# Optimization experiments

Measured on AMD Instinct MI355X. Metric: run time of the kernel, lower is better.

The kernel has to match this reference:

```python
import jax, jax.numpy as jnp
import numpy as np

N_GROUPS = 32  # getGroupSize(.) assumed -> channels // 8 (or //24 for 3*ch) == 32 for ch=256
HEADS = 4


def group_norm(x, gamma, beta, groups=N_GROUPS, eps=1e-5):
    n, c = x.shape
    xg = x.reshape(n, groups, c // groups)
    mu = xg.mean(-1, keepdims=True)
    var = xg.var(-1, keepdims=True)
    xn = ((xg - mu) * jax.lax.rsqrt(var + eps)).reshape(n, c)
    return xn * gamma + beta


def setup_inputs():
    key = jax.random.key(0)
    N, E, CH, HID = 2000, 16000, 256, 256
    ks = jax.random.split(key, 24)

    def w(k, shape, s=0.02):
        return (jax.random.normal(k, shape) * s).astype(jnp.float32)

    inp = {
        'x': jax.random.normal(ks[0], (N, CH), jnp.float32),
        'edge_index': jax.random.randint(ks[1], (2, E), 0, N),
        'edge_attr': jax.random.normal(ks[2], (E, CH), jnp.float32),
        # edge_mlp: GN(3ch)+ReLU -> Linear(3ch,hid) -> GN(hid)+ReLU -> Linear(hid,ch)
        'gn_e1_g': jnp.ones((3 * CH,), jnp.float32), 'gn_e1_b': jnp.zeros((3 * CH,), jnp.float32),
        'We1': w(ks[3], (3 * CH, HID)), 'be1': jnp.zeros((HID,), jnp.float32),
        'gn_e2_g': jnp.ones((HID,), jnp.float32), 'gn_e2_b': jnp.zeros((HID,), jnp.float32),
        'We2': w(ks[4], (HID, CH)), 'be2': jnp.zeros((CH,), jnp.float32),
        # actN: GN(ch)+ReLU
        'gn_n_g': jnp.ones((CH,), jnp.float32), 'gn_n_b': jnp.zeros((CH,), jnp.float32),
        # multi-head attention projections
        'Wq': w(ks[5], (CH, CH)), 'bq': jnp.zeros((CH,), jnp.float32),
        'Wk': w(ks[6], (CH, CH)), 'bk': jnp.zeros((CH,), jnp.float32),
        'Wv': w(ks[7], (CH, CH)), 'bv': jnp.zeros((CH,), jnp.float32),
        'Wo': w(ks[8], (CH, CH)), 'bo': jnp.zeros((CH,), jnp.float32),
        # node_mlp: Linear(2ch,hid) -> GN(hid)+ReLU -> Linear(hid,ch)
        'Wn1': w(ks[9], (2 * CH, HID)), 'bn1': jnp.zeros((HID,), jnp.float32),
        'gn_n2_g': jnp.ones((HID,), jnp.float32), 'gn_n2_b': jnp.zeros((HID,), jnp.float32),
        'Wn2': w(ks[10], (HID, CH)), 'bn2': jnp.zeros((CH,), jnp.float32),
    }
    return inp


def reference(x, edge_index, edge_attr,
              gn_e1_g, gn_e1_b, We1, be1, gn_e2_g, gn_e2_b, We2, be2,
              gn_n_g, gn_n_b, Wq, bq, Wk, bk, Wv, bv, Wo, bo,
              Wn1, bn1, gn_n2_g, gn_n2_b, Wn2, bn2):
    row, col = edge_index[0], edge_index[1]
    N, ch = x.shape
    E = edge_attr.shape[0]
    dk = ch // HEADS

    # ---- edge model: cat(src, tgt, e) -> GN/ReLU -> Lin -> GN/ReLU -> Lin (+res) ----
    e_in = jnp.concatenate([x[row], x[col], edge_attr], axis=1)  # [E, 3ch]
    h = jax.nn.relu(group_norm(e_in, gn_e1_g, gn_e1_b))
    h = h @ We1 + be1
    h = jax.nn.relu(group_norm(h, gn_e2_g, gn_e2_b))
    e_out = h @ We2 + be2 + edge_attr  # [E, ch]

    # ---- node model: dense-masked MHA, queries=nodes, keys/values=edges ----
    mask = jnp.zeros((N, E), x.dtype).at[col, jnp.arange(E)].set(1.0)  # scatter adjacency
    q = (x @ Wq + bq).reshape(N, HEADS, dk)
    k = (e_out @ Wk + bk).reshape(E, HEADS, dk)
    v = (e_out @ Wv + bv).reshape(E, HEADS, dk)
    scores = jnp.einsum('nhd,ehd->hne', q, k) / jnp.sqrt(jnp.float32(dk))  # [H, N, E]
    scores = jnp.where(mask[None] > 0, scores, jnp.float32(-1e9))
    attn = jax.nn.softmax(scores, axis=-1)
    g = jnp.einsum('hne,ehd->nhd', attn, v).reshape(N, ch) @ Wo + bo  # [N, ch]

    xa = jax.nn.relu(group_norm(x, gn_n_g, gn_n_b))
    h = jnp.concatenate([xa, g], axis=1) @ Wn1 + bn1  # thinker='cat'
    h = jax.nn.relu(group_norm(h, gn_n2_g, gn_n2_b))
    n_out = h @ Wn2 + bn2 + x  # residual

    return n_out, e_out
```

## Files before the change

kernel.cpp:

```cpp
#include <hip/hip_runtime.h>
#include <hip/hip_bf16.h>
#include <stdint.h>
#include <math.h>

#define CH 256

typedef __attribute__((ext_vector_type(8)))  short short8;
typedef __attribute__((ext_vector_type(16))) short short16;
typedef __attribute__((ext_vector_type(4)))  float f32x4;

#define GL2LDS16(g, l) __builtin_amdgcn_global_load_lds(                       \
    (const __attribute__((address_space(1))) void*)(g),                        \
    (__attribute__((address_space(3))) void*)(l), 16, 0, 0)

__device__ inline short f2bf(float f) {
    __hip_bfloat16 h = __float2bfloat16(f);
    short s;
    __builtin_memcpy(&s, &h, 2);
    return s;
}

__device__ inline float warp_sum64(float v) {
    v += __shfl_xor(v, 32, 64);
    v += __shfl_xor(v, 16, 64);
    v += __shfl_xor(v, 8, 64);
    v += __shfl_xor(v, 4, 64);
    v += __shfl_xor(v, 2, 64);
    v += __shfl_xor(v, 1, 64);
    return v;
}

template <int BM, int BN, int EPI, int VB>
__global__ __launch_bounds__(256) void mfma_gemm(
    const short* __restrict__ A, const short* __restrict__ Bt,
    const float* __restrict__ bias, const float* __restrict__ res,
    float* __restrict__ C, short* __restrict__ Cbf,
    const float* __restrict__ gamma, const float* __restrict__ beta,
    float* __restrict__ vbar,
    int M, int K, int Nc, int ldc, int coff)
{
    constexpr int BK = 32;
    constexpr int HM = BM / 2, HN = BN / 2;
    constexpr int FM = HM / 16, FN = HN / 16;
    constexpr int PA = (BM * BK) / (256 * 8);
    constexpr int PB = (BN * BK) / (256 * 8);
    __shared__ short As[BM * BK];
    __shared__ short Bs[BN * BK];

    const int t = threadIdx.x;
    const int wave = t >> 6, lane = t & 63;
    const int q = lane >> 4, l16 = lane & 15;
    const int row0 = blockIdx.y * BM;
    const int col0 = blockIdx.x * BN;
    const int wm = wave & 1, wn = wave >> 1;

    f32x4 acc[FM][FN];
    #pragma unroll
    for (int i = 0; i < FM; i++)
        #pragma unroll
        for (int j = 0; j < FN; j++) acc[i][j] = (f32x4){0.f, 0.f, 0.f, 0.f};

    for (int k0 = 0; k0 < K; k0 += BK) {
        #pragma unroll
        for (int p = 0; p < PA; p++) {
            int chunk = p * 256 + t;
            int r = chunk >> 2, ko = (chunk & 3) * 8;
            int gr = row0 + r; if (gr >= M) gr = M - 1;
            const short* gsrc = A + (size_t)gr * K + k0 + ko;
            short* ldst = &As[(p * 256 + wave * 64) * 8];
            GL2LDS16(gsrc, ldst);
        }
        #pragma unroll
        for (int p = 0; p < PB; p++) {
            int chunk = p * 256 + t;
            int r = chunk >> 2, ko = (chunk & 3) * 8;
            const short* gsrc = Bt + (size_t)(col0 + r) * K + k0 + ko;
            short* ldst = &Bs[(p * 256 + wave * 64) * 8];
            GL2LDS16(gsrc, ldst);
        }
        __syncthreads();
        short8 af[FM], bf[FN];
        #pragma unroll
        for (int mi = 0; mi < FM; mi++)
            af[mi] = *(const short8*)&As[(wm * HM + mi * 16 + l16) * BK + q * 8];
        #pragma unroll
        for (int ni = 0; ni < FN; ni++)
            bf[ni] = *(const short8*)&Bs[(wn * HN + ni * 16 + l16) * BK + q * 8];
        #pragma unroll
        for (int mi = 0; mi < FM; mi++)
            #pragma unroll
            for (int ni = 0; ni < FN; ni++)
                acc[mi][ni] = __builtin_amdgcn_mfma_f32_16x16x32_bf16(
                    af[mi], bf[ni], acc[mi][ni], 0, 0, 0);
        __syncthreads();
    }

    #pragma unroll
    for (int ni = 0; ni < FN; ni++) {
        int cg = col0 + wn * HN + ni * 16 + l16;
        float bv = bias[cg];
        if constexpr (EPI == 1) {
            float ga = gamma[cg], be = beta[cg];
            #pragma unroll
            for (int mi = 0; mi < FM; mi++) {
                #pragma unroll
                for (int r = 0; r < 4; r++) {
                    float v = acc[mi][ni][r] + bv;
                    float s = v, sq = v * v;
                    s += __shfl_xor(s, 1, 64);  sq += __shfl_xor(sq, 1, 64);
                    s += __shfl_xor(s, 2, 64);  sq += __shfl_xor(sq, 2, 64);
                    s += __shfl_xor(s, 4, 64);  sq += __shfl_xor(sq, 4, 64);
                    float mean = s * 0.125f;
                    float var = sq * 0.125f - mean * mean;
                    float o = fmaxf((v - mean) * rsqrtf(var + 1e-5f) * ga + be, 0.f);
                    int rg = row0 + wm * HM + mi * 16 + q * 4 + r;
                    if (rg < M) Cbf[(size_t)rg * ldc + coff + cg] = f2bf(o);
                }
            }
        } else {
            #pragma unroll
            for (int mi = 0; mi < FM; mi++) {
                #pragma unroll
                for (int r = 0; r < 4; r++) {
                    int rg = row0 + wm * HM + mi * 16 + q * 4 + r;
                    if (rg < M) {
                        float v = acc[mi][ni][r] + bv;
                        if (res) v += res[(size_t)rg * ldc + coff + cg];
                        if (C)   C[(size_t)rg * ldc + coff + cg] = v;
                        if (Cbf) Cbf[(size_t)rg * ldc + coff + cg] = f2bf(v);
                    }
                }
            }
            if constexpr (VB) {
                if (cg >= 256) {
                    float part = 0.f;
                    #pragma unroll
                    for (int mi = 0; mi < FM; mi++)
                        #pragma unroll
                        for (int r = 0; r < 4; r++) {
                            int rg = row0 + wm * HM + mi * 16 + q * 4 + r;
                            if (rg < M) part += acc[mi][ni][r] + bv;
                        }
                    part += __shfl_xor(part, 16, 64);
                    part += __shfl_xor(part, 32, 64);
                    if (q == 0) atomicAdd(&vbar[cg - 256], part);
                }
            }
        }
    }
}

struct WPack {
    const float* src[8];
    short* dst[8];
    int K[8];
    int start[8];
};

__global__ __launch_bounds__(256) void wconv_kernel(WPack p)
{
    int gk = blockIdx.x;
    int m = 0;
    #pragma unroll
    for (int i = 1; i < 8; i++) if (gk >= p.start[i]) m = i;
    int k0 = (gk - p.start[m]) * 16;
    int t = threadIdx.x;
    const float* src = p.src[m];
    short16 o;
    #pragma unroll
    for (int j = 0; j < 16; j++) o[j] = f2bf(src[(size_t)(k0 + j) * 256 + t]);
    *(short16*)(p.dst[m] + (size_t)t * p.K[m] + k0) = o;
}

__global__ __launch_bounds__(256) void prep_kernel(
    const float* __restrict__ x, short* __restrict__ x_bf,
    short* __restrict__ cat_bf,
    const float* __restrict__ gng, const float* __restrict__ gnb,
    float* __restrict__ vbar, const float* __restrict__ bk,
    const float* __restrict__ bv, float* __restrict__ bkv, int N)
{
    int t = threadIdx.x;
    if (blockIdx.x == 0) {
        vbar[t] = 0.f;
        bkv[t] = bk[t];
        bkv[256 + t] = bv[t];
    }
    int r = blockIdx.x * 8 + (t >> 5);
    int g = t & 31;
    if (r >= N) return;
    size_t xb = (size_t)r * CH + g * 8;
    float4 a = *(const float4*)&x[xb];
    float4 b = *(const float4*)&x[xb + 4];
    short8 xr;
    xr[0] = f2bf(a.x); xr[1] = f2bf(a.y); xr[2] = f2bf(a.z); xr[3] = f2bf(a.w);
    xr[4] = f2bf(b.x); xr[5] = f2bf(b.y); xr[6] = f2bf(b.z); xr[7] = f2bf(b.w);
    *(short8*)&x_bf[xb] = xr;
    float s  = a.x + a.y + a.z + a.w + b.x + b.y + b.z + b.w;
    float s2 = a.x*a.x + a.y*a.y + a.z*a.z + a.w*a.w
             + b.x*b.x + b.y*b.y + b.z*b.z + b.w*b.w;
    float m = s * 0.125f;
    float var = s2 * 0.125f - m * m;
    float rsd = rsqrtf(var + 1e-5f);
    float4 g0 = *(const float4*)&gng[g * 8];
    float4 g1 = *(const float4*)&gng[g * 8 + 4];
    float4 b0 = *(const float4*)&gnb[g * 8];
    float4 b1 = *(const float4*)&gnb[g * 8 + 4];
    short8 o;
    o[0] = f2bf(fmaxf((a.x - m) * rsd * g0.x + b0.x, 0.f));
    o[1] = f2bf(fmaxf((a.y - m) * rsd * g0.y + b0.y, 0.f));
    o[2] = f2bf(fmaxf((a.z - m) * rsd * g0.z + b0.z, 0.f));
    o[3] = f2bf(fmaxf((a.w - m) * rsd * g0.w + b0.w, 0.f));
    o[4] = f2bf(fmaxf((b.x - m) * rsd * g1.x + b1.x, 0.f));
    o[5] = f2bf(fmaxf((b.y - m) * rsd * g1.y + b1.y, 0.f));
    o[6] = f2bf(fmaxf((b.z - m) * rsd * g1.z + b1.z, 0.f));
    o[7] = f2bf(fmaxf((b.w - m) * rsd * g1.w + b1.w, 0.f));
    *(short8*)&cat_bf[(size_t)r * (2 * CH) + g * 8] = o;
}

__global__ __launch_bounds__(256) void build_ein_kernel(
    const float* __restrict__ x, const float* __restrict__ eattr,
    const int* __restrict__ rowi, const int* __restrict__ coli,
    const float* __restrict__ gng, const float* __restrict__ gnb,
    short* __restrict__ ein, int E)
{
    __shared__ float sb[768];
    __shared__ float smu[32], srs[32];
    int e = blockIdx.x, t = threadIdx.x;
    int r = rowi[e], c = coli[e];
    float v0 = x[(size_t)r * CH + t];
    float v1 = x[(size_t)c * CH + t];
    float v2 = eattr[(size_t)e * CH + t];
    sb[t] = v0; sb[256 + t] = v1; sb[512 + t] = v2;
    __syncthreads();
    if (t < 32) {
        float s = 0.f, s2 = 0.f;
        const float* p = &sb[t * 24];
        #pragma unroll
        for (int i = 0; i < 24; i++) { float v = p[i]; s += v; s2 += v * v; }
        float m = s * (1.f / 24.f);
        float var = s2 * (1.f / 24.f) - m * m;
        smu[t] = m; srs[t] = rsqrtf(var + 1e-5f);
    }
    __syncthreads();
    size_t base = (size_t)e * 768;
    #pragma unroll
    for (int j = 0; j < 3; j++) {
        int pos = j * 256 + t;
        int g = pos / 24;
        float v = (j == 0) ? v0 : (j == 1) ? v1 : v2;
        v = fmaxf((v - smu[g]) * srs[g] * gng[pos] + gnb[pos], 0.f);
        ein[base + pos] = f2bf(v);
    }
}

__global__ __launch_bounds__(1024) void csr_kernel(
    const int* __restrict__ coli, int* __restrict__ offsets,
    int* __restrict__ elist, int N, int E)
{
    __shared__ int cnt[2048];
    __shared__ int s[1024];
    int t = threadIdx.x;
    cnt[t] = 0; cnt[1024 + t] = 0;
    __syncthreads();
    for (int e = t; e < E; e += 1024) atomicAdd(&cnt[coli[e]], 1);
    __syncthreads();
    int a = (2 * t     < N) ? cnt[2 * t]     : 0;
    int b = (2 * t + 1 < N) ? cnt[2 * t + 1] : 0;
    s[t] = a + b;
    __syncthreads();
    for (int off = 1; off < 1024; off <<= 1) {
        int v = (t >= off) ? s[t - off] : 0;
        __syncthreads();
        s[t] += v;
        __syncthreads();
    }
    int excl = (t > 0) ? s[t - 1] : 0;
    if (2 * t < N)     { offsets[2 * t]     = excl;     cnt[2 * t]     = excl; }
    if (2 * t + 1 < N) { offsets[2 * t + 1] = excl + a; cnt[2 * t + 1] = excl + a; }
    if (t == 1023) offsets[N] = s[1023];
    __syncthreads();
    for (int e = t; e < E; e += 1024) {
        int p = atomicAdd(&cnt[coli[e]], 1);
        elist[p] = e;
    }
}

__global__ __launch_bounds__(256) void attn_kernel(
    const float* __restrict__ qb, const float* __restrict__ kv,
    const int* __restrict__ offsets, const int* __restrict__ elist,
    const float* __restrict__ vbar, short* __restrict__ g_bf, int N, int E)
{
    int n = blockIdx.x;
    int c = threadIdx.x;
    float qv = qb[(size_t)n * CH + c];
    int s0 = offsets[n], s1 = offsets[n + 1];
    float out;
    if (s1 > s0) {
        float m = -INFINITY, l = 0.f, num = 0.f;
        int e = elist[s0];
        float kc = kv[(size_t)e * 512 + c];
        float vc = kv[(size_t)e * 512 + 256 + c];
        for (int idx = s0; idx < s1; idx++) {
            float kcur = kc, vcur = vc;
            if (idx + 1 < s1) {
                int e2 = elist[idx + 1];
                kc = kv[(size_t)e2 * 512 + c];
                vc = kv[(size_t)e2 * 512 + 256 + c];
            }
            float sdot = warp_sum64(qv * kcur) * 0.125f;
            float mn = fmaxf(m, sdot);
            float sc = __expf(m - mn);
            float p  = __expf(sdot - mn);
            l = l * sc + p;
            num = num * sc + p * vcur;
            m = mn;
        }
        out = num / l;
    } else {
        out = vbar[c] * (1.f / (float)E);
    }
    g_bf[(size_t)n * CH + c] = f2bf(out);
}

extern "C" void kernel_launch(void* const* d_in, const int* in_sizes, int n_in,
                              void* d_out, int out_size, void* d_ws, size_t ws_size,
                              hipStream_t stream)
{
    const float* x       = (const float*)d_in[0];
    const int*   ei      = (const int*)d_in[1];
    const float* eattr   = (const float*)d_in[2];
    const float* gn_e1_g = (const float*)d_in[3];
    const float* gn_e1_b = (const float*)d_in[4];
    const float* We1     = (const float*)d_in[5];
    const float* be1     = (const float*)d_in[6];
    const float* gn_e2_g = (const float*)d_in[7];
    const float* gn_e2_b = (const float*)d_in[8];
    const float* We2     = (const float*)d_in[9];
    const float* be2     = (const float*)d_in[10];
    const float* gn_n_g  = (const float*)d_in[11];
    const float* gn_n_b  = (const float*)d_in[12];
    const float* Wq      = (const float*)d_in[13];
    const float* bq      = (const float*)d_in[14];
    const float* Wk      = (const float*)d_in[15];
    const float* bk      = (const float*)d_in[16];
    const float* Wv      = (const float*)d_in[17];
    const float* bv      = (const float*)d_in[18];
    const float* Wo      = (const float*)d_in[19];
    const float* bo      = (const float*)d_in[20];
    const float* Wn1     = (const float*)d_in[21];
    const float* bn1     = (const float*)d_in[22];
    const float* gn_n2_g = (const float*)d_in[23];
    const float* gn_n2_b = (const float*)d_in[24];
    const float* Wn2     = (const float*)d_in[25];
    const float* bn2     = (const float*)d_in[26];

    const int N = in_sizes[0] / CH;
    const int E = in_sizes[2] / CH;

    float* nout = (float*)d_out;
    float* eout = (float*)d_out + (size_t)N * CH;

    char* base = (char*)d_ws;
    short* ein_bf = (short*)base;
    float* kvbuf  = (float*)base;
    base += (size_t)E * 512 * 4;
    short* h2_bf  = (short*)base; base += (size_t)E * CH * 2;
    short* eo_bf  = (short*)base; base += (size_t)E * CH * 2;
    float* qbuf   = (float*)base; base += (size_t)N * CH * 4;
    short* g_bf   = (short*)base; base += (size_t)N * CH * 2;
    short* cat_bf = (short*)base; base += (size_t)N * 2 * CH * 2;
    short* hn_bf  = (short*)base; base += (size_t)N * CH * 2;
    short* x_bf   = (short*)base; base += (size_t)N * CH * 2;
    float* vbar   = (float*)base; base += 1024;
    float* bkv    = (float*)base; base += 2048;
    short* We1t = (short*)base; base += (size_t)768 * 256 * 2;
    short* We2t = (short*)base; base += (size_t)256 * 256 * 2;
    short* Wqt  = (short*)base; base += (size_t)256 * 256 * 2;
    short* Wkvt = (short*)base; base += (size_t)512 * 256 * 2;
    short* Wot  = (short*)base; base += (size_t)256 * 256 * 2;
    short* Wn1t = (short*)base; base += (size_t)512 * 256 * 2;
    short* Wn2t = (short*)base; base += (size_t)256 * 256 * 2;
    int* offsets = (int*)base;
    int* elist   = offsets + (N + 1) + 3;

    const int* rowi = ei;
    const int* coli = ei + E;

    dim3 blk(256);
    dim3 gE(CH / 64, E / 128);
    dim3 gKV(512 / 64, E / 128);
    dim3 gN(CH / 64, (N + 63) / 64);

    WPack wp;
    const float* wsrc[8] = {We1, We2, Wq, Wk, Wv, Wo, Wn1, Wn2};
    short* wdst[8] = {We1t, We2t, Wqt, Wkvt, Wkvt + (size_t)256 * 256, Wot, Wn1t, Wn2t};
    const int wKd[8] = {768, 256, 256, 256, 256, 256, 512, 256};
    int acc = 0;
    for (int i = 0; i < 8; i++) {
        wp.src[i] = wsrc[i]; wp.dst[i] = wdst[i]; wp.K[i] = wKd[i];
        wp.start[i] = acc; acc += wKd[i] / 16;
    }
    wconv_kernel<<<acc, blk, 0, stream>>>(wp);
    prep_kernel<<<(N + 7) / 8, blk, 0, stream>>>(x, x_bf, cat_bf, gn_n_g, gn_n_b,
                                                 vbar, bk, bv, bkv, N);
    csr_kernel<<<1, 1024, 0, stream>>>(coli, offsets, elist, N, E);

    build_ein_kernel<<<E, blk, 0, stream>>>(x, eattr, rowi, coli, gn_e1_g, gn_e1_b, ein_bf, E);
    mfma_gemm<128, 64, 1, 0><<<gE, blk, 0, stream>>>(
        ein_bf, We1t, be1, nullptr, nullptr, h2_bf, gn_e2_g, gn_e2_b, nullptr,
        E, 3 * CH, CH, CH, 0);
    mfma_gemm<128, 64, 0, 0><<<gE, blk, 0, stream>>>(
        h2_bf, We2t, be2, eattr, eout, eo_bf, nullptr, nullptr, nullptr,
        E, CH, CH, CH, 0);

    mfma_gemm<128, 64, 0, 1><<<gKV, blk, 0, stream>>>(
        eo_bf, Wkvt, bkv, nullptr, kvbuf, nullptr, nullptr, nullptr, vbar,
        E, CH, 512, 512, 0);
    mfma_gemm<64, 64, 0, 0><<<gN, blk, 0, stream>>>(
        x_bf, Wqt, bq, nullptr, qbuf, nullptr, nullptr, nullptr, nullptr,
        N, CH, CH, CH, 0);

    attn_kernel<<<N, blk, 0, stream>>>(qbuf, kvbuf, offsets, elist, vbar, g_bf, N, E);
    mfma_gemm<64, 64, 0, 0><<<gN, blk, 0, stream>>>(
        g_bf, Wot, bo, nullptr, nullptr, cat_bf, nullptr, nullptr, nullptr,
        N, CH, CH, 2 * CH, CH);

    mfma_gemm<64, 64, 1, 0><<<gN, blk, 0, stream>>>(
        cat_bf, Wn1t, bn1, nullptr, nullptr, hn_bf, gn_n2_g, gn_n2_b, nullptr,
        N, 2 * CH, CH, CH, 0);
    mfma_gemm<64, 64, 0, 0><<<gN, blk, 0, stream>>>(
        hn_bf, Wn2t, bn2, x, nout, nullptr, nullptr, nullptr, nullptr,
        N, CH, CH, CH, 0);
}
```

Measured before the change: 277.6 us.

## Parallelize CSR build, precompute edge scores, widen GEMM K tile, merge prep kernels

Several changes land together. The GEMM K tile doubles to 64, with two MFMA sub-steps per tile, and the KV GEMM uses a 128x128 tile. The single-block CSR build is replaced by per-edge atomic counting inside build_ein, a scan kernel and a parallel fill kernel, and weight conversion is merged into the prep kernel. Attention now precomputes per-edge, per-head scores in a separate kernel and does a chunked online softmax over 64 edges at a time, instead of a serial per-edge warp reduction. These target the serial CSR bottleneck and latency-bound attention, at the cost of extra launches and a non-deterministic elist order from the atomics.

Result: faster. 267.2 us (-3.7%).

```diff
diff --git a/kernel.cpp b/kernel.cpp
--- a/kernel.cpp
+++ b/kernel.cpp
@@ -30,6 +30,16 @@
     return v;
 }
 
+__device__ inline float warp_max64(float v) {
+    v = fmaxf(v, __shfl_xor(v, 32, 64));
+    v = fmaxf(v, __shfl_xor(v, 16, 64));
+    v = fmaxf(v, __shfl_xor(v, 8, 64));
+    v = fmaxf(v, __shfl_xor(v, 4, 64));
+    v = fmaxf(v, __shfl_xor(v, 2, 64));
+    v = fmaxf(v, __shfl_xor(v, 1, 64));
+    return v;
+}
+
 template <int BM, int BN, int EPI, int VB>
 __global__ __launch_bounds__(256) void mfma_gemm(
     const short* __restrict__ A, const short* __restrict__ Bt,
@@ -39,7 +49,7 @@
     float* __restrict__ vbar,
     int M, int K, int Nc, int ldc, int coff)
 {
-    constexpr int BK = 32;
+    constexpr int BK = 64;
     constexpr int HM = BM / 2, HN = BN / 2;
     constexpr int FM = HM / 16, FN = HN / 16;
     constexpr int PA = (BM * BK) / (256 * 8);
@@ -64,7 +74,7 @@
         #pragma unroll
         for (int p = 0; p < PA; p++) {
             int chunk = p * 256 + t;
-            int r = chunk >> 2, ko = (chunk & 3) * 8;
+            int r = chunk >> 3, ko = (chunk & 7) * 8;
             int gr = row0 + r; if (gr >= M) gr = M - 1;
             const short* gsrc = A + (size_t)gr * K + k0 + ko;
             short* ldst = &As[(p * 256 + wave * 64) * 8];
@@ -73,25 +83,28 @@
         #pragma unroll
         for (int p = 0; p < PB; p++) {
             int chunk = p * 256 + t;
-            int r = chunk >> 2, ko = (chunk & 3) * 8;
+            int r = chunk >> 3, ko = (chunk & 7) * 8;
             const short* gsrc = Bt + (size_t)(col0 + r) * K + k0 + ko;
             short* ldst = &Bs[(p * 256 + wave * 64) * 8];
             GL2LDS16(gsrc, ldst);
         }
         __syncthreads();
-        short8 af[FM], bf[FN];
-        #pragma unroll
-        for (int mi = 0; mi < FM; mi++)
-            af[mi] = *(const short8*)&As[(wm * HM + mi * 16 + l16) * BK + q * 8];
-        #pragma unroll
-        for (int ni = 0; ni < FN; ni++)
-            bf[ni] = *(const short8*)&Bs[(wn * HN + ni * 16 + l16) * BK + q * 8];
-        #pragma unroll
-        for (int mi = 0; mi < FM; mi++)
+        #pragma unroll
+        for (int ks = 0; ks < 2; ks++) {
+            short8 af[FM], bf[FN];
+            #pragma unroll
+            for (int mi = 0; mi < FM; mi++)
+                af[mi] = *(const short8*)&As[(wm * HM + mi * 16 + l16) * BK + ks * 32 + q * 8];
             #pragma unroll
             for (int ni = 0; ni < FN; ni++)
-                acc[mi][ni] = __builtin_amdgcn_mfma_f32_16x16x32_bf16(
-                    af[mi], bf[ni], acc[mi][ni], 0, 0, 0);
+                bf[ni] = *(const short8*)&Bs[(wn * HN + ni * 16 + l16) * BK + ks * 32 + q * 8];
+            #pragma unroll
+            for (int mi = 0; mi < FM; mi++)
+                #pragma unroll
+                for (int ni = 0; ni < FN; ni++)
+                    acc[mi][ni] = __builtin_amdgcn_mfma_f32_16x16x32_bf16(
+                        af[mi], bf[ni], acc[mi][ni], 0, 0, 0);
+        }
         __syncthreads();
     }
 
@@ -150,61 +163,72 @@
     }
 }
 
-struct WPack {
-    const float* src[8];
-    short* dst[8];
-    int K[8];
-    int start[8];
+struct PrepPack {
+    const float* wsrc[8];
+    short* wdst[8];
+    int wK[8];
+    int wstart[8];
+    int NW, NP;
+    const float* x;
+    short* x_bf;
+    short* cat_bf;
+    const float* gng;
+    const float* gnb;
+    float* vbar;
+    const float* bk;
+    const float* bv;
+    float* bkv;
+    int* counts;
+    int N;
 };
 
-__global__ __launch_bounds__(256) void wconv_kernel(WPack p)
-{
-    int gk = blockIdx.x;
-    int m = 0;
-    #pragma unroll
-    for (int i = 1; i < 8; i++) if (gk >= p.start[i]) m = i;
-    int k0 = (gk - p.start[m]) * 16;
+__global__ __launch_bounds__(256) void prep_kernel(PrepPack p)
+{
+    int bid = blockIdx.x;
     int t = threadIdx.x;
-    const float* src = p.src[m];
-    short16 o;
-    #pragma unroll
-    for (int j = 0; j < 16; j++) o[j] = f2bf(src[(size_t)(k0 + j) * 256 + t]);
-    *(short16*)(p.dst[m] + (size_t)t * p.K[m] + k0) = o;
-}
-
-__global__ __launch_bounds__(256) void prep_kernel(
-    const float* __restrict__ x, short* __restrict__ x_bf,
-    short* __restrict__ cat_bf,
-    const float* __restrict__ gng, const float* __restrict__ gnb,
-    float* __restrict__ vbar, const float* __restrict__ bk,
-    const float* __restrict__ bv, float* __restrict__ bkv, int N)
-{
-    int t = threadIdx.x;
-    if (blockIdx.x == 0) {
-        vbar[t] = 0.f;
-        bkv[t] = bk[t];
-        bkv[256 + t] = bv[t];
-    }
-    int r = blockIdx.x * 8 + (t >> 5);
+    if (bid < p.NW) {
+        int m = 0;
+        #pragma unroll
+        for (int i = 1; i < 8; i++) if (bid >= p.wstart[i]) m = i;
+        int k0 = (bid - p.wstart[m]) * 16;
+        const float* src = p.wsrc[m];
+        short16 o;
+        #pragma unroll
+        for (int j = 0; j < 16; j++) o[j] = f2bf(src[(size_t)(k0 + j) * 256 + t]);
+        *(short16*)(p.wdst[m] + (size_t)t * p.wK[m] + k0) = o;
+        return;
+    }
+    if (bid >= p.NW + p.NP) {
+        int i = (bid - p.NW - p.NP) * 256 + t;
+        if (i < p.N) p.counts[i] = 0;
+        return;
+    }
+    int pb = bid - p.NW;
+    if (pb == 0) {
+        p.vbar[t] = 0.f;
+        p.bkv[t] = p.bk[t];
+        p.bkv[256 + t] = p.bv[t];
+    }
+    int r = pb * 8 + (t >> 5);
     int g = t & 31;
-    if (r >= N) return;
+    if (r >= p.N) return;
     size_t xb = (size_t)r * CH + g * 8;
-    float4 a = *(const float4*)&x[xb];
-    float4 b = *(const float4*)&x[xb + 4];
+    float4 a = *(const float4*)&p.x[xb];
+    float4 b = *(const float4*)&p.x[xb + 4];
     short8 xr;
     xr[0] = f2bf(a.x); xr[1] = f2bf(a.y); xr[2] = f2bf(a.z); xr[3] = f2bf(a.w);
     xr[4] = f2bf(b.x); xr[5] = f2bf(b.y); xr[6] = f2bf(b.z); xr[7] = f2bf(b.w);
-    *(short8*)&x_bf[xb] = xr;
+    *(short8*)&p.x_bf[xb] = xr;
     float s  = a.x + a.y + a.z + a.w + b.x + b.y + b.z + b.w;
     float s2 = a.x*a.x + a.y*a.y + a.z*a.z + a.w*a.w
              + b.x*b.x + b.y*b.y + b.z*b.z + b.w*b.w;
     float m = s * 0.125f;
     float var = s2 * 0.125f - m * m;
     float rsd = rsqrtf(var + 1e-5f);
-    float4 g0 = *(const float4*)&gng[g * 8];
-    float4 g1 = *(const float4*)&gng[g * 8 + 4];
-    float4 b0 = *(const float4*)&gnb[g * 8];
-    float4 b1 = *(const float4*)&gnb[g * 8 + 4];
+    float4 g0 = *(const float4*)&p.gng[g * 8];
+    float4 g1 = *(const float4*)&p.gng[g * 8 + 4];
+    float4 b0 = *(const float4*)&p.gnb[g * 8];
+    float4 b1 = *(const float4*)&p.gnb[g * 8 + 4];
     short8 o;
     o[0] = f2bf(fmaxf((a.x - m) * rsd * g0.x + b0.x, 0.f));
     o[1] = f2bf(fmaxf((a.y - m) * rsd * g0.y + b0.y, 0.f));
@@ -214,19 +238,20 @@
     o[5] = f2bf(fmaxf((b.y - m) * rsd * g1.y + b1.y, 0.f));
     o[6] = f2bf(fmaxf((b.z - m) * rsd * g1.z + b1.z, 0.f));
     o[7] = f2bf(fmaxf((b.w - m) * rsd * g1.w + b1.w, 0.f));
-    *(short8*)&cat_bf[(size_t)r * (2 * CH) + g * 8] = o;
+    *(short8*)&p.cat_bf[(size_t)r * (2 * CH) + g * 8] = o;
 }
 
 __global__ __launch_bounds__(256) void build_ein_kernel(
     const float* __restrict__ x, const float* __restrict__ eattr,
     const int* __restrict__ rowi, const int* __restrict__ coli,
     const float* __restrict__ gng, const float* __restrict__ gnb,
-    short* __restrict__ ein, int E)
+    short* __restrict__ ein, int* __restrict__ counts, int E)
 {
     __shared__ float sb[768];
     __shared__ float smu[32], srs[32];
     int e = blockIdx.x, t = threadIdx.x;
     int r = rowi[e], c = coli[e];
+    if (t == 0) atomicAdd(&counts[c], 1);
     float v0 = x[(size_t)r * CH + t];
     float v1 = x[(size_t)c * CH + t];
     float v2 = eattr[(size_t)e * CH + t];
@@ -253,19 +278,14 @@
     }
 }
 
-__global__ __launch_bounds__(1024) void csr_kernel(
-    const int* __restrict__ coli, int* __restrict__ offsets,
-    int* __restrict__ elist, int N, int E)
-{
-    __shared__ int cnt[2048];
+__global__ __launch_bounds__(1024) void scan_kernel(
+    const int* __restrict__ counts, int* __restrict__ offsets,
+    int* __restrict__ cursor, int N)
+{
     __shared__ int s[1024];
     int t = threadIdx.x;
-    cnt[t] = 0; cnt[1024 + t] = 0;
-    __syncthreads();
-    for (int e = t; e < E; e += 1024) atomicAdd(&cnt[coli[e]], 1);
-    __syncthreads();
-    int a = (2 * t     < N) ? cnt[2 * t]     : 0;
-    int b = (2 * t + 1 < N) ? cnt[2 * t + 1] : 0;
+    int a = (2 * t     < N) ? counts[2 * t]     : 0;
+    int b = (2 * t + 1 < N) ? counts[2 * t + 1] : 0;
     s[t] = a + b;
     __syncthreads();
     for (int off = 1; off < 1024; off <<= 1) {
@@ -275,51 +295,80 @@
         __syncthreads();
     }
     int excl = (t > 0) ? s[t - 1] : 0;
-    if (2 * t < N)     { offsets[2 * t]     = excl;     cnt[2 * t]     = excl; }
-    if (2 * t + 1 < N) { offsets[2 * t + 1] = excl + a; cnt[2 * t + 1] = excl + a; }
+    if (2 * t < N)     { offsets[2 * t]     = excl;     cursor[2 * t]     = excl; }
+    if (2 * t + 1 < N) { offsets[2 * t + 1] = excl + a; cursor[2 * t + 1] = excl + a; }
     if (t == 1023) offsets[N] = s[1023];
-    __syncthreads();
-    for (int e = t; e < E; e += 1024) {
-        int p = atomicAdd(&cnt[coli[e]], 1);
+}
+
+__global__ void fill_kernel(const int* __restrict__ coli, int* __restrict__ cursor,
+                            int* __restrict__ elist, int E)
+{
+    int e = blockIdx.x * blockDim.x + threadIdx.x;
+    if (e < E) {
+        int p = atomicAdd(&cursor[coli[e]], 1);
         elist[p] = e;
     }
 }
 
+__global__ __launch_bounds__(256) void escore_kernel(
+    const float* __restrict__ qb, const float* __restrict__ kv,
+    const int* __restrict__ coli, float* __restrict__ sc, int E)
+{
+    int e = blockIdx.x * 4 + (threadIdx.x >> 6);
+    int lane = threadIdx.x & 63;
+    if (e >= E) return;
+    int c = coli[e];
+    const float* qrow = qb + (size_t)c * CH;
+    const float* krow = kv + (size_t)e * 512;
+    float d0 = qrow[lane]       * krow[lane];
+    float d1 = qrow[64 + lane]  * krow[64 + lane];
+    float d2 = qrow[128 + lane] * krow[128 + lane];
+    float d3 = qrow[192 + lane] * krow[192 + lane];
+    d0 = warp_sum64(d0);
+    d1 = warp_sum64(d1);
+    d2 = warp_sum64(d2);
+    d3 = warp_sum64(d3);
+    if (lane == 0) {
+        float4 o = {d0 * 0.125f, d1 * 0.125f, d2 * 0.125f, d3 * 0.125f};
+        *(float4*)&sc[(size_t)e * 4] = o;
+    }
+}
+
 __global__ __launch_bounds__(256) void attn_kernel(
-    const float* __restrict__ qb, const float* __restrict__ kv,
+    const float* __restrict__ sc, const float* __restrict__ kv,
     const int* __restrict__ offsets, const int* __restrict__ elist,
     const float* __restrict__ vbar, short* __restrict__ g_bf, int N, int E)
 {
     int n = blockIdx.x;
-    int c = threadIdx.x;
-    float qv = qb[(size_t)n * CH + c];
+    int h = threadIdx.x >> 6;
+    int lane = threadIdx.x & 63;
     int s0 = offsets[n], s1 = offsets[n + 1];
-    float out;
+    float out = 0.f;
     if (s1 > s0) {
-        float m = -INFINITY, l = 0.f, num = 0.f;
-        int e = elist[s0];
-        float kc = kv[(size_t)e * 512 + c];
-        float vc = kv[(size_t)e * 512 + 256 + c];
-        for (int idx = s0; idx < s1; idx++) {
-            float kcur = kc, vcur = vc;
-            if (idx + 1 < s1) {
-                int e2 = elist[idx + 1];
-                kc = kv[(size_t)e2 * 512 + c];
-                vc = kv[(size_t)e2 * 512 + 256 + c];
+        float m = -INFINITY, l = 0.f;
+        for (int base = s0; base < s1; base += 64) {
+            int cn = s1 - base; if (cn > 64) cn = 64;
+            int e = (lane < cn) ? elist[base + lane] : 0;
+            float s = (lane < cn) ? sc[(size_t)e * 4 + h] : -INFINITY;
+            float mc = warp_max64(s);
+            float nm = fmaxf(m, mc);
+            float scale = __expf(m - nm);
+            float pp = (lane < cn) ? __expf(s - nm) : 0.f;
+            float ps = warp_sum64(pp);
+            l = l * scale + ps;
+            out *= scale;
+            m = nm;
+            for (int i = 0; i < cn; i++) {
+                float pi = __shfl(pp, i, 64);
+                int   ei = __shfl(e, i, 64);
+                out += pi * kv[(size_t)ei * 512 + 256 + h * 64 + lane];
             }
-            float sdot = warp_sum64(qv * kcur) * 0.125f;
-            float mn = fmaxf(m, sdot);
-            float sc = __expf(m - mn);
-            float p  = __expf(sdot - mn);
-            l = l * sc + p;
-            num = num * sc + p * vcur;
-            m = mn;
         }
-        out = num / l;
+        out /= l;
     } else {
-        out = vbar[c] * (1.f / (float)E);
-    }
-    g_bf[(size_t)n * CH + c] = f2bf(out);
+        out = vbar[h * 64 + lane] * (1.f / (float)E);
+    }
+    g_bf[(size_t)n * CH + h * 64 + lane] = f2bf(out);
 }
 
 extern "C" void kernel_launch(void* const* d_in, const int* in_sizes, int n_in,
@@ -371,6 +420,7 @@
     short* cat_bf = (short*)base; base += (size_t)N * 2 * CH * 2;
     short* hn_bf  = (short*)base; base += (size_t)N * CH * 2;
     short* x_bf   = (short*)base; base += (size_t)N * CH * 2;
+    float* sc     = (float*)base; base += (size_t)E * 4 * 4;
     float* vbar   = (float*)base; base += 1024;
     float* bkv    = (float*)base; base += 2048;
     short* We1t = (short*)base; base += (size_t)768 * 256 * 2;
@@ -380,32 +430,42 @@
     short* Wot  = (short*)base; base += (size_t)256 * 256 * 2;
     short* Wn1t = (short*)base; base += (size_t)512 * 256 * 2;
     short* Wn2t = (short*)base; base += (size_t)256 * 256 * 2;
-    int* offsets = (int*)base;
-    int* elist   = offsets + (N + 1) + 3;
+    int* counts  = (int*)base;
+    int* offsets = counts + N;
+    int* cursor  = offsets + (N + 1) + 3;
+    int* elist   = cursor + N;
 
     const int* rowi = ei;
     const int* coli = ei + E;
 
     dim3 blk(256);
     dim3 gE(CH / 64, E / 128);
-    dim3 gKV(512 / 64, E / 128);
+    dim3 gKV(512 / 128, E / 128);
     dim3 gN(CH / 64, (N + 63) / 64);
 
-    WPack wp;
+    PrepPack pp;
     const float* wsrc[8] = {We1, We2, Wq, Wk, Wv, Wo, Wn1, Wn2};
     short* wdst[8] = {We1t, We2t, Wqt, Wkvt, Wkvt + (size_t)256 * 256, Wot, Wn1t, Wn2t};
     const int wKd[8] = {768, 256, 256, 256, 256, 256, 512, 256};
     int acc = 0;
     for (int i = 0; i < 8; i++) {
-        wp.src[i] = wsrc[i]; wp.dst[i] = wdst[i]; wp.K[i] = wKd[i];
-        wp.start[i] = acc; acc += wKd[i] / 16;
-    }
-    wconv_kernel<<<acc, blk, 0, stream>>>(wp);
-    prep_kernel<<<(N + 7) / 8, blk, 0, stream>>>(x, x_bf, cat_bf, gn_n_g, gn_n_b,
-                                                 vbar, bk, bv, bkv, N);
-    csr_kernel<<<1, 1024, 0, stream>>>(coli, offsets, elist, N, E);
-
-    build_ein_kernel<<<E, blk, 0, stream>>>(x, eattr, rowi, coli, gn_e1_g, gn_e1_b, ein_bf, E);
+        pp.wsrc[i] = wsrc[i]; pp.wdst[i] = wdst[i]; pp.wK[i] = wKd[i];
+        pp.wstart[i] = acc; acc += wKd[i] / 16;
+    }
+    pp.NW = acc;
+    pp.NP = (N + 7) / 8;
+    pp.x = x; pp.x_bf = x_bf; pp.cat_bf = cat_bf;
+    pp.gng = gn_n_g; pp.gnb = gn_n_b;
+    pp.vbar = vbar; pp.bk = bk; pp.bv = bv; pp.bkv = bkv;
+    pp.counts = counts; pp.N = N;
+    int nzero = (N + 255) / 256;
+    prep_kernel<<<pp.NW + pp.NP + nzero, blk, 0, stream>>>(pp);
+
+    build_ein_kernel<<<E, blk, 0, stream>>>(x, eattr, rowi, coli, gn_e1_g, gn_e1_b,
+                                            ein_bf, counts, E);
+    scan_kernel<<<1, 1024, 0, stream>>>(counts, offsets, cursor, N);
+    fill_kernel<<<(E + 255) / 256, blk, 0, stream>>>(coli, cursor, elist, E);
+
     mfma_gemm<128, 64, 1, 0><<<gE, blk, 0, stream>>>(
         ein_bf, We1t, be1, nullptr, nullptr, h2_bf, gn_e2_g, gn_e2_b, nullptr,
         E, 3 * CH, CH, CH, 0);
@@ -413,14 +473,15 @@
         h2_bf, We2t, be2, eattr, eout, eo_bf, nullptr, nullptr, nullptr,
         E, CH, CH, CH, 0);
 
-    mfma_gemm<128, 64, 0, 1><<<gKV, blk, 0, stream>>>(
+    mfma_gemm<128, 128, 0, 1><<<gKV, blk, 0, stream>>>(
         eo_bf, Wkvt, bkv, nullptr, kvbuf, nullptr, nullptr, nullptr, vbar,
         E, CH, 512, 512, 0);
     mfma_gemm<64, 64, 0, 0><<<gN, blk, 0, stream>>>(
         x_bf, Wqt, bq, nullptr, qbuf, nullptr, nullptr, nullptr, nullptr,
         N, CH, CH, CH, 0);
 
-    attn_kernel<<<N, blk, 0, stream>>>(qbuf, kvbuf, offsets, elist, vbar, g_bf, N, E);
+    escore_kernel<<<(E + 3) / 4, blk, 0, stream>>>(qbuf, kvbuf, coli, sc, E);
+    attn_kernel<<<N, blk, 0, stream>>>(sc, kvbuf, offsets, elist, vbar, g_bf, N, E);
     mfma_gemm<64, 64, 0, 0><<<gN, blk, 0, stream>>>(
         g_bf, Wot, bo, nullptr, nullptr, cat_bf, nullptr, nullptr, nullptr,
         N, CH, CH, 2 * CH, CH);
```
